# Kernel tuning notes

Measured on AMD Instinct MI355X. Metric: run time of the kernel, lower is better.

The kernel has to match this reference:

```python
import jax, jax.numpy as jnp
import numpy as np

B, S, D, H = 2, 2048, 1024, 16
DK = D // H


def setup_inputs() -> dict:
    key = jax.random.key(0)
    ks = jax.random.split(key, 12)
    scale = 1.0 / np.sqrt(D)
    inp = {
        "q": jax.random.normal(ks[0], (B, S, D), jnp.float32),
        "k": jax.random.normal(ks[1], (B, S, D), jnp.float32),
        "v": jax.random.normal(ks[2], (B, S, D), jnp.float32),
        # causal mask: 1 = attend, 0 = mask, broadcastable to (B, 1, S, S)
        "mask": jnp.tril(jnp.ones((S, S), jnp.int32))[None, None, :, :],
        "Wq": jax.random.normal(ks[3], (D, D), jnp.float32) * scale,
        "bq": jax.random.normal(ks[4], (D,), jnp.float32) * scale,
        "Wk": jax.random.normal(ks[5], (D, D), jnp.float32) * scale,
        "bk": jax.random.normal(ks[6], (D,), jnp.float32) * scale,
        "Wv": jax.random.normal(ks[7], (D, D), jnp.float32) * scale,
        "bv": jax.random.normal(ks[8], (D,), jnp.float32) * scale,
        "Wo": jax.random.normal(ks[9], (D, D), jnp.float32) * scale,
        "bo": jax.random.normal(ks[10], (D,), jnp.float32) * scale,
    }
    return inp


def _split_heads(x):
    b, s, _ = x.shape
    return x.reshape(b, s, H, DK).transpose(0, 2, 1, 3)  # (b, h, s, dk)


def reference(q, k, v, mask, Wq, bq, Wk, bk, Wv, bv, Wo, bo):
    Q = _split_heads(q @ Wq.T + bq)
    K = _split_heads(k @ Wk.T + bk)
    V = _split_heads(v @ Wv.T + bv)
    scores = jnp.einsum("bhqd,bhkd->bhqk", Q, K) * (DK ** -0.5)
    scores = jnp.where(mask == 0, -jnp.inf, scores)
    attn = jax.nn.softmax(scores, axis=-1)  # dropout p=0.0 -> identity
    out = jnp.einsum("bhqk,bhkd->bhqd", attn, V)
    out = out.transpose(0, 2, 1, 3).reshape(q.shape[0], q.shape[1], D)
    return out @ Wo.T + bo
```

## Files before the change

### kernel.cpp

```cpp
#include <hip/hip_runtime.h>


#define S_LEN 2048
#define NHEAD 16
#define DMODEL 1024
#define DKH 64
#define LDT 88

typedef unsigned short u16;
typedef __attribute__((ext_vector_type(4))) short short4v;
typedef __attribute__((ext_vector_type(8))) short short8;
typedef __attribute__((ext_vector_type(8))) __bf16 bf16x8;
typedef __attribute__((ext_vector_type(4))) float f32x4;

__device__ inline u16 f2bf(float f) {
  return __builtin_bit_cast(u16, (__bf16)f);
}

__device__ inline f32x4 mfma16x16(bf16x8 a, bf16x8 b, f32x4 c) {
  return __builtin_amdgcn_mfma_f32_16x16x32_bf16(a, b, c, 0, 0, 0);
}

__device__ inline short8 pack8(float4 a, float4 b) {
  short8 r;
  r[0] = (short)f2bf(a.x); r[1] = (short)f2bf(a.y);
  r[2] = (short)f2bf(a.z); r[3] = (short)f2bf(a.w);
  r[4] = (short)f2bf(b.x); r[5] = (short)f2bf(b.y);
  r[6] = (short)f2bf(b.z); r[7] = (short)f2bf(b.w);
  return r;
}

typedef const __attribute__((address_space(1))) unsigned GU32;
typedef __attribute__((address_space(3))) unsigned LU32;
__device__ inline void gl2lds16(const void* g, void* l) {
  __builtin_amdgcn_global_load_lds((GU32*)g, (LU32*)l, 16, 0, 0);
}

#define SWZ(row, col8) (((row) * 8 + ((col8) ^ ((row) & 7))) * 8)

__global__ __launch_bounds__(256)
void conv_w(const float* __restrict__ w0, const float* __restrict__ w1,
            const float* __restrict__ w2, const float* __restrict__ w3,
            u16* __restrict__ o0, u16* __restrict__ o1,
            u16* __restrict__ o2, u16* __restrict__ o3)
{
  const int z = blockIdx.y;
  const float* s = z == 0 ? w0 : z == 1 ? w1 : z == 2 ? w2 : w3;
  u16* d = z == 0 ? o0 : z == 1 ? o1 : z == 2 ? o2 : o3;
  const int i = (blockIdx.x * 256 + threadIdx.x) * 8;
  float4 a = *(const float4*)&s[i];
  float4 b = *(const float4*)&s[i + 4];
  *(short8*)&d[i] = pack8(a, b);
}

__global__ __launch_bounds__(256)
void proj_gemm(const float* __restrict__ Aq, const float* __restrict__ Akk,
               const float* __restrict__ Av,
               const u16* __restrict__ Bq, const u16* __restrict__ Bk,
               const u16* __restrict__ Bv,
               const float* __restrict__ cq, const float* __restrict__ ck,
               const float* __restrict__ cv,
               u16* __restrict__ Oq, u16* __restrict__ Ok, u16* __restrict__ Ov)
{
  __shared__ u16 SM[3 * 128 * 64];
  u16* As = SM;
  u16* Bs0 = SM + 8192;
  u16* Bs1 = SM + 16384;

  const int hw = blockIdx.x + (blockIdx.y << 3) + (blockIdx.z << 8);
  const int xcd = hw & 7, sq = hw >> 3;
  const int pan = sq % 12, xb = sq / 12;
  const int p = pan * 8 + xcd;
  const int zz = p >> 5, py = p & 31;

  const float* Af = zz == 0 ? Aq : zz == 1 ? Akk : Av;
  const u16* Wb = zz == 0 ? Bq : zz == 1 ? Bk : Bv;
  const float* bias = zz == 0 ? cq : zz == 1 ? ck : cv;

  const int t = threadIdx.x;
  const int lane = t & 63;
  const int wv = t >> 6;
  const int wm = wv >> 1, wn = wv & 1;
  const int g = lane >> 4, lr = lane & 15;
  const int bm = py << 7, bn = xb << 7;
  const int K = DMODEL;

  float4 ax[4], ay[4];
  auto ALOAD = [&](int kt) {
    const int k0 = kt << 6;
#pragma unroll
    for (int i = 0; i < 4; ++i) {
      int c = t + (i << 8);
      int row = c >> 3, col8 = c & 7;
      const float* src = &Af[(size_t)(bm + row) * K + k0 + col8 * 8];
      ax[i] = *(const float4*)src;
      ay[i] = *(const float4*)(src + 4);
    }
  };
  auto AWRITE = [&]() {
#pragma unroll
    for (int i = 0; i < 4; ++i) {
      int c = t + (i << 8);
      int row = c >> 3, col8 = c & 7;
      *(short8*)&As[SWZ(row, col8)] = pack8(ax[i], ay[i]);
    }
  };
  auto BSTAGE = [&](u16* buf, int kt) {
    const int k0 = kt << 6;
#pragma unroll
    for (int i = 0; i < 4; ++i) {
      int c = t + (i << 8);
      int row = c >> 3, col8 = c & 7;
      int c8s = col8 ^ (row & 7);
      gl2lds16(&Wb[(size_t)(bn + row) * K + k0 + c8s * 8], &buf[c * 8]);
    }
  };

  f32x4 acc[4][4] = {};
  ALOAD(0);
  BSTAGE(Bs0, 0);
  AWRITE();
  __syncthreads();
  for (int kt = 0; kt < 16; ++kt) {
    u16* Bcur = (kt & 1) ? Bs1 : Bs0;
    u16* Bnxt = (kt & 1) ? Bs0 : Bs1;
    const bool more = (kt + 1 < 16);
    if (more) { ALOAD(kt + 1); BSTAGE(Bnxt, kt + 1); }
    bf16x8 af[2][4], bf[2][4];
#pragma unroll
    for (int kc = 0; kc < 2; ++kc)
#pragma unroll
      for (int f = 0; f < 4; ++f) {
        af[kc][f] = *(const bf16x8*)&As[SWZ(wm * 64 + f * 16 + lr, kc * 4 + g)];
        bf[kc][f] = *(const bf16x8*)&Bcur[SWZ(wn * 64 + f * 16 + lr, kc * 4 + g)];
      }
#pragma unroll
    for (int kc = 0; kc < 2; ++kc)
#pragma unroll
      for (int fm = 0; fm < 4; ++fm)
#pragma unroll
        for (int fn = 0; fn < 4; ++fn)
          acc[fm][fn] = mfma16x16(af[kc][fm], bf[kc][fn], acc[fm][fn]);
    __syncthreads();
    if (more) {
      AWRITE();
      __syncthreads();
    }
  }

  if (zz == 2) {
    u16* TL = SM;
    const int b = bm >> 11, s0 = bm & (S_LEN - 1), h0 = bn >> 6;
#pragma unroll
    for (int hh = 0; hh < 2; ++hh) {
      __syncthreads();
      if (wn == hh) {
#pragma unroll
        for (int fm = 0; fm < 4; ++fm)
#pragma unroll
          for (int fn = 0; fn < 4; ++fn) {
            const int lch = fn * 16 + lr;
            const float bb = bias[bn + hh * 64 + lch];
#pragma unroll
            for (int r = 0; r < 4; ++r)
              TL[lch * 132 + wm * 64 + fm * 16 + g * 4 + r] = f2bf(acc[fm][fn][r] + bb);
          }
      }
      __syncthreads();
#pragma unroll
      for (int i = 0; i < 4; ++i) {
        int c = t + (i << 8);
        int dk = c >> 4, sc = (c & 15) << 3;
        short8 vv = *(const short8*)&TL[dk * 132 + sc];
        *(short8*)&Ov[(((size_t)(b * NHEAD + h0 + hh)) * DKH + dk) * S_LEN + s0 + sc] = vv;
      }
    }
  } else {
    u16* Out = zz == 0 ? Oq : Ok;
#pragma unroll
    for (int fm = 0; fm < 4; ++fm)
#pragma unroll
      for (int fn = 0; fn < 4; ++fn) {
        const int col = bn + wn * 64 + fn * 16 + lr;
        const int h = col >> 6, dk = col & (DKH - 1);
        const float bb = bias[col];
#pragma unroll
        for (int r = 0; r < 4; ++r) {
          const int row = bm + wm * 64 + fm * 16 + g * 4 + r;
          const int b = row >> 11, s = row & (S_LEN - 1);
          Out[(((size_t)(b * NHEAD + h)) * S_LEN + s) * DKH + dk] = f2bf(acc[fm][fn][r] + bb);
        }
      }
  }
}

__global__ __launch_bounds__(256)
void out_gemm(const u16* __restrict__ Ao, const u16* __restrict__ Wb,
              const float* __restrict__ bias, float* __restrict__ Out)
{
  __shared__ u16 SM[4 * 128 * 64];
  const int hw = blockIdx.x + (blockIdx.y << 3);
  const int xcd = hw & 7, sq = hw >> 3;
  const int pan = sq & 3, xb = sq >> 2;
  const int prow = pan * 8 + xcd;

  const int t = threadIdx.x;
  const int lane = t & 63;
  const int wv = t >> 6;
  const int wm = wv >> 1, wn = wv & 1;
  const int g = lane >> 4, lr = lane & 15;
  const int bm = prow << 7, bn = xb << 7;
  const int K = DMODEL;

  auto STAGE = [&](int buf, int kt) {
    const int k0 = kt << 6;
    u16* Asb = SM + buf * 8192;
    u16* Bsb = SM + 16384 + buf * 8192;
#pragma unroll
    for (int i = 0; i < 4; ++i) {
      int c = t + (i << 8);
      int row = c >> 3, col8 = c & 7;
      int c8s = col8 ^ (row & 7);
      int grow = bm + row;
      int b = grow >> 11, s = grow & (S_LEN - 1);
      int k = k0 + c8s * 8;
      int h = k >> 6, dk = k & (DKH - 1);
      gl2lds16(&Ao[(((size_t)(b * NHEAD + h)) * S_LEN + s) * DKH + dk], &Asb[c * 8]);
      gl2lds16(&Wb[(size_t)(bn + row) * K + k0 + c8s * 8], &Bsb[c * 8]);
    }
  };

  f32x4 acc[4][4] = {};
  STAGE(0, 0);
  __syncthreads();
  for (int kt = 0; kt < 16; ++kt) {
    const int cur = kt & 1;
    if (kt + 1 < 16) STAGE(cur ^ 1, kt + 1);
    u16* Asb = SM + cur * 8192;
    u16* Bsb = SM + 16384 + cur * 8192;
    bf16x8 af[2][4], bf[2][4];
#pragma unroll
    for (int kc = 0; kc < 2; ++kc)
#pragma unroll
      for (int f = 0; f < 4; ++f) {
        af[kc][f] = *(const bf16x8*)&Asb[SWZ(wm * 64 + f * 16 + lr, kc * 4 + g)];
        bf[kc][f] = *(const bf16x8*)&Bsb[SWZ(wn * 64 + f * 16 + lr, kc * 4 + g)];
      }
#pragma unroll
    for (int kc = 0; kc < 2; ++kc)
#pragma unroll
      for (int fm = 0; fm < 4; ++fm)
#pragma unroll
        for (int fn = 0; fn < 4; ++fn)
          acc[fm][fn] = mfma16x16(af[kc][fm], bf[kc][fn], acc[fm][fn]);
    __syncthreads();
  }
#pragma unroll
  for (int fm = 0; fm < 4; ++fm)
#pragma unroll
    for (int fn = 0; fn < 4; ++fn) {
      const int col = bn + wn * 64 + fn * 16 + lr;
      const float bb = bias[col];
#pragma unroll
      for (int r = 0; r < 4; ++r) {
        const int row = bm + wm * 64 + fm * 16 + g * 4 + r;
        Out[(size_t)row * DMODEL + col] = acc[fm][fn][r] + bb;
      }
    }
}

template<bool AF32, int OMODE>
__global__ __launch_bounds__(256)
void gemm64(const void* __restrict__ Ap, const float* __restrict__ Bt,
            const float* __restrict__ bias, void* __restrict__ outp,
            int M, int N, int K)
{
  __shared__ u16 As[64 * LDT];
  __shared__ u16 Bs[64 * LDT];
  const int t = threadIdx.x;
  const int lane = t & 63;
  const int wv = t >> 6;
  const int wm = wv >> 1, wn = wv & 1;
  const int g = lane >> 4, lr = lane & 15;
  const int bm = blockIdx.y << 6, bn = blockIdx.x << 6;

  f32x4 acc[2][2] = {};
  const int nk = K >> 6;
  for (int kt = 0; kt < nk; ++kt) {
    const int k0 = kt << 6;
    __syncthreads();
#pragma unroll
    for (int i = 0; i < 2; ++i) {
      int c = t + (i << 8);
      int row = c >> 3, col = (c & 7) << 3;
      short8 av;
      if (AF32) {
        const float* Af = (const float*)Ap;
        const float4* pa = (const float4*)&Af[(size_t)(bm + row) * K + k0 + col];
        av = pack8(pa[0], pa[1]);
      } else {
        av = *(const short8*)&((const u16*)Ap)[(size_t)(bm + row) * K + k0 + col];
      }
      *(short8*)&As[row * LDT + col] = av;
      const float4* pb = (const float4*)&Bt[(size_t)(bn + row) * K + k0 + col];
      *(short8*)&Bs[row * LDT + col] = pack8(pb[0], pb[1]);
    }
    __syncthreads();
    bf16x8 af[2][2], bfr[2][2];
#pragma unroll
    for (int kc = 0; kc < 2; ++kc) {
#pragma unroll
      for (int fm = 0; fm < 2; ++fm)
        af[kc][fm] = *(const bf16x8*)&As[(wm * 32 + fm * 16 + lr) * LDT + kc * 32 + g * 8];
#pragma unroll
      for (int fn = 0; fn < 2; ++fn)
        bfr[kc][fn] = *(const bf16x8*)&Bs[(wn * 32 + fn * 16 + lr) * LDT + kc * 32 + g * 8];
    }
#pragma unroll
    for (int kc = 0; kc < 2; ++kc)
#pragma unroll
      for (int fm = 0; fm < 2; ++fm)
#pragma unroll
        for (int fn = 0; fn < 2; ++fn)
          acc[fm][fn] = mfma16x16(af[kc][fm], bfr[kc][fn], acc[fm][fn]);
  }
  if (OMODE == 2) {
    u16* TL = As;
    __syncthreads();
#pragma unroll
    for (int fm = 0; fm < 2; ++fm)
#pragma unroll
      for (int fn = 0; fn < 2; ++fn) {
        const int lc = wn * 32 + fn * 16 + lr;
        const float bb = bias[bn + lc];
#pragma unroll
        for (int r = 0; r < 4; ++r) {
          const int lrow = wm * 32 + fm * 16 + g * 4 + r;
          TL[lc * LDT + lrow] = f2bf(acc[fm][fn][r] + bb);
        }
      }
    __syncthreads();
    const int bh = (bm >> 11) * NHEAD + (bn >> 6);
    const int s0 = bm & (S_LEN - 1);
#pragma unroll
    for (int i = 0; i < 2; ++i) {
      int c = t + (i << 8);
      int dr = c >> 3, sc = (c & 7) << 3;
      short8 vv = *(const short8*)&TL[dr * LDT + sc];
      *(short8*)&((u16*)outp)[((size_t)bh * DKH + dr) * S_LEN + s0 + sc] = vv;
    }
  } else {
#pragma unroll
    for (int fm = 0; fm < 2; ++fm)
#pragma unroll
      for (int fn = 0; fn < 2; ++fn) {
        const int col = bn + wn * 32 + fn * 16 + lr;
        const float bb = bias[col];
#pragma unroll
        for (int r = 0; r < 4; ++r) {
          const int row = bm + wm * 32 + fm * 16 + g * 4 + r;
          float vv = acc[fm][fn][r] + bb;
          if (OMODE == 1) {
            int b = row >> 11, s = row & (S_LEN - 1);
            int h = col >> 6, dk = col & (DKH - 1);
            ((u16*)outp)[(((size_t)(b * NHEAD + h)) * S_LEN + s) * DKH + dk] = f2bf(vv);
          } else {
            ((float*)outp)[(size_t)row * N + col] = vv;
          }
        }
      }
  }
}

template<bool HS>
__global__ __launch_bounds__(256)
void attn_fwd(const u16* __restrict__ Qh, const u16* __restrict__ Kh,
              const u16* __restrict__ Vtg, u16* __restrict__ Ao)
{
  __shared__ u16 Ks[2][64 * LDT];
  __shared__ u16 Vs[2][64 * LDT];
  __shared__ u16 Ps[8][16 * LDT];
  const int t = threadIdx.x, lane = t & 63, w = t >> 6;
  const int g = lane >> 4, lr = lane & 15;
  const int bh = blockIdx.y;
  const int pA = blockIdx.x;
  const int tA = pA, tB = 31 - pA;
  const u16* Qb = Qh + (size_t)bh * S_LEN * DKH;
  const u16* Kb = Kh + (size_t)bh * S_LEN * DKH;
  const u16* Vb = Vtg + (size_t)bh * DKH * S_LEN;

  bf16x8 qfA[2], qfB[2];
#pragma unroll
  for (int kc = 0; kc < 2; ++kc) {
    qfA[kc] = *(const bf16x8*)&Qb[(size_t)(tA * 64 + w * 16 + lr) * DKH + kc * 32 + g * 8];
    qfB[kc] = *(const bf16x8*)&Qb[(size_t)(tB * 64 + w * 16 + lr) * DKH + kc * 32 + g * 8];
  }

  f32x4 oA[4] = {}, oB[4] = {};
  float mA = -1e30f, lA = 0.f, mB = -1e30f, lB = 0.f;

  const int r0 = t >> 3;
  const int c0 = (t & 7) << 3;
  short8 kr0, kr1, vr0, vr1;

  auto LOADT = [&](int kt) {
    const int kv0 = kt << 6;
    kr0 = *(const short8*)&Kb[(size_t)(kv0 + r0) * DKH + c0];
    kr1 = *(const short8*)&Kb[(size_t)(kv0 + r0 + 32) * DKH + c0];
    vr0 = *(const short8*)&Vb[(size_t)r0 * S_LEN + kv0 + c0];
    vr1 = *(const short8*)&Vb[(size_t)(r0 + 32) * S_LEN + kv0 + c0];
  };
  auto WRITET = [&](int b) {
    *(short8*)&Ks[b][r0 * LDT + c0] = kr0;
    *(short8*)&Ks[b][(r0 + 32) * LDT + c0] = kr1;
    *(short8*)&Vs[b][r0 * LDT + c0] = vr0;
    *(short8*)&Vs[b][(r0 + 32) * LDT + c0] = vr1;
  };

  auto COMPUTE = [&](int buf, const bf16x8* qf, f32x4* o, float& m, float& l,
                     int pslot, bool diag) {
    f32x4 sf[4];
#pragma unroll
    for (int fk = 0; fk < 4; ++fk) {
      f32x4 a = {};
#pragma unroll
      for (int kc = 0; kc < 2; ++kc) {
        bf16x8 kf = *(const bf16x8*)&Ks[buf][(fk * 16 + lr) * LDT + kc * 32 + g * 8];
        a = mfma16x16(kf, qf[kc], a);
      }
      sf[fk] = a;
    }
    if (diag) {
#pragma unroll
      for (int fk = 0; fk < 4; ++fk)
#pragma unroll
        for (int r = 0; r < 4; ++r)
          if (fk * 16 + 4 * g + r > w * 16 + lr) sf[fk][r] = -1e30f;
    }
    float pm = fmaxf(fmaxf(sf[0][0], sf[0][1]), fmaxf(sf[0][2], sf[0][3]));
#pragma unroll
    for (int fk = 1; fk < 4; ++fk)
      pm = fmaxf(pm, fmaxf(fmaxf(sf[fk][0], sf[fk][1]), fmaxf(sf[fk][2], sf[fk][3])));
    pm = fmaxf(pm, __shfl_xor(pm, 16, 64));
    pm = fmaxf(pm, __shfl_xor(pm, 32, 64));
    float alpha = 1.0f;
    if (!__all(pm - m <= 64.0f)) {
      float mn = fmaxf(m, pm);
      alpha = __expf((m - mn) * 0.125f);
      m = mn;
#pragma unroll
      for (int r = 0; r < 4; ++r) {
        float ar = __shfl(alpha, 4 * g + r, 64);
#pragma unroll
        for (int d = 0; d < 4; ++d) o[d][r] *= ar;
      }
    }
    float rs = 0.f;
#pragma unroll
    for (int fk = 0; fk < 4; ++fk) {
      float p0 = __expf((sf[fk][0] - m) * 0.125f);
      float p1 = __expf((sf[fk][1] - m) * 0.125f);
      float p2 = __expf((sf[fk][2] - m) * 0.125f);
      float p3 = __expf((sf[fk][3] - m) * 0.125f);
      rs += (p0 + p1) + (p2 + p3);
      short4v pk;
      pk[0] = (short)f2bf(p0); pk[1] = (short)f2bf(p1);
      pk[2] = (short)f2bf(p2); pk[3] = (short)f2bf(p3);
      *(short4v*)&Ps[pslot][lr * LDT + fk * 16 + 4 * g] = pk;
    }
    rs += __shfl_xor(rs, 16, 64);
    rs += __shfl_xor(rs, 32, 64);
    l = l * alpha + rs;
#pragma unroll
    for (int kc = 0; kc < 2; ++kc) {
      bf16x8 pf = *(const bf16x8*)&Ps[pslot][lr * LDT + kc * 32 + g * 8];
#pragma unroll
      for (int df = 0; df < 4; ++df) {
        bf16x8 vf = *(const bf16x8*)&Vs[buf][(df * 16 + lr) * LDT + kc * 32 + g * 8];
        o[df] = mfma16x16(pf, vf, o[df]);
      }
    }
  };

  const int nt = tB + 1;
  LOADT(0);
  WRITET(0);
  for (int kt = 0; kt < nt; ++kt) {
    const int cur = kt & 1;
    const bool more = (kt + 1 < nt);
    if (more) LOADT(kt + 1);
    __syncthreads();
    if (kt <= tA) COMPUTE(cur, qfA, oA, mA, lA, w, kt == tA);
    COMPUTE(cur, qfB, oB, mB, lB, 4 + w, kt == tB);
    if (more) WRITET(cur ^ 1);
  }

  float iA[4], iB[4];
#pragma unroll
  for (int r = 0; r < 4; ++r) {
    iA[r] = __builtin_amdgcn_rcpf(__shfl(lA, 4 * g + r, 64));
    iB[r] = __builtin_amdgcn_rcpf(__shfl(lB, 4 * g + r, 64));
  }
  const int b = bh >> 4, h = bh & (NHEAD - 1);
#pragma unroll
  for (int df = 0; df < 4; ++df)
#pragma unroll
    for (int r = 0; r < 4; ++r) {
      const int d = df * 16 + lr;
      const int qa = tA * 64 + w * 16 + g * 4 + r;
      const int qb2 = tB * 64 + w * 16 + g * 4 + r;
      if (HS) {
        Ao[((size_t)bh * S_LEN + qa) * DKH + d] = f2bf(oA[df][r] * iA[r]);
        Ao[((size_t)bh * S_LEN + qb2) * DKH + d] = f2bf(oB[df][r] * iB[r]);
      } else {
        Ao[((size_t)(b * S_LEN + qa)) * DMODEL + h * DKH + d] = f2bf(oA[df][r] * iA[r]);
        Ao[((size_t)(b * S_LEN + qb2)) * DMODEL + h * DKH + d] = f2bf(oB[df][r] * iB[r]);
      }
    }
}

extern "C" void kernel_launch(void* const* d_in, const int* in_sizes, int n_in,
                              void* d_out, int out_size, void* d_ws, size_t ws_size,
                              hipStream_t stream)
{
  (void)in_sizes; (void)n_in; (void)out_size;
  const float* q  = (const float*)d_in[0];
  const float* k  = (const float*)d_in[1];
  const float* v  = (const float*)d_in[2];
  const float* Wq = (const float*)d_in[4];
  const float* bq = (const float*)d_in[5];
  const float* Wk = (const float*)d_in[6];
  const float* bk = (const float*)d_in[7];
  const float* Wv = (const float*)d_in[8];
  const float* bv = (const float*)d_in[9];
  const float* Wo = (const float*)d_in[10];
  const float* bo = (const float*)d_in[11];

  char* ws = (char*)d_ws;
  const size_t MB = 1024 * 1024;

  if (ws_size >= 40 * MB) {
    u16* Wqb = (u16*)(ws);
    u16* Wkb = (u16*)(ws + 2 * MB);
    u16* Wvb = (u16*)(ws + 4 * MB);
    u16* Wob = (u16*)(ws + 6 * MB);
    u16* Qh  = (u16*)(ws + 8 * MB);
    u16* Kh  = (u16*)(ws + 16 * MB);
    u16* Vt  = (u16*)(ws + 24 * MB);
    u16* Ao  = (u16*)(ws + 32 * MB);

    conv_w<<<dim3(512, 4), 256, 0, stream>>>(Wq, Wk, Wv, Wo, Wqb, Wkb, Wvb, Wob);
    proj_gemm<<<dim3(8, 32, 3), 256, 0, stream>>>(q, k, v, Wqb, Wkb, Wvb,
                                                  bq, bk, bv, Qh, Kh, Vt);
    attn_fwd<true><<<dim3(16, 2 * NHEAD), 256, 0, stream>>>(Qh, Kh, Vt, Ao);
    out_gemm<<<dim3(8, 32), 256, 0, stream>>>(Ao, Wob, bo, (float*)d_out);
  } else {
    u16* Qh = (u16*)(ws);
    u16* Kh = (u16*)(ws + 8 * MB);
    u16* Vt = (u16*)(ws + 16 * MB);
    u16* Ao = (u16*)(ws + 24 * MB);
    const int M = 2 * S_LEN, N = DMODEL, K = DMODEL;
    dim3 gg(N / 64, M / 64), bb(256);
    gemm64<true, 1><<<gg, bb, 0, stream>>>(q, Wq, bq, Qh, M, N, K);
    gemm64<true, 1><<<gg, bb, 0, stream>>>(k, Wk, bk, Kh, M, N, K);
    gemm64<true, 2><<<gg, bb, 0, stream>>>(v, Wv, bv, Vt, M, N, K);
    attn_fwd<false><<<dim3(16, 2 * NHEAD), bb, 0, stream>>>(Qh, Kh, Vt, Ao);
    gemm64<false, 0><<<gg, bb, 0, stream>>>(Ao, Wo, bo, d_out, M, N, K);
  }
}
```

Measured before the change: 131.7 us.

## Pre-convert activations to bf16 and use async LDS-loading projection GEMM

```diff
diff --git a/kernel.cpp b/kernel.cpp
--- a/kernel.cpp
+++ b/kernel.cpp
@@ -37,6 +37,33 @@
 }
 
 #define SWZ(row, col8) (((row) * 8 + ((col8) ^ ((row) & 7))) * 8)
+
+__global__ __launch_bounds__(256)
+void conv_bf16(const float* __restrict__ w0, const float* __restrict__ w1,
+               const float* __restrict__ w2, const float* __restrict__ w3,
+               const float* __restrict__ aq, const float* __restrict__ ak,
+               const float* __restrict__ av,
+               u16* __restrict__ o0, u16* __restrict__ o1,
+               u16* __restrict__ o2, u16* __restrict__ o3,
+               u16* __restrict__ oq, u16* __restrict__ ok, u16* __restrict__ ov)
+{
+  const int y = blockIdx.y;
+  const float* s; u16* d; int n;
+  switch (y) {
+    case 0: s = w0; d = o0; n = 1 << 20; break;
+    case 1: s = w1; d = o1; n = 1 << 20; break;
+    case 2: s = w2; d = o2; n = 1 << 20; break;
+    case 3: s = w3; d = o3; n = 1 << 20; break;
+    case 4: s = aq; d = oq; n = 1 << 22; break;
+    case 5: s = ak; d = ok; n = 1 << 22; break;
+    default: s = av; d = ov; n = 1 << 22; break;
+  }
+  const int i = (blockIdx.x * 256 + threadIdx.x) * 8;
+  if (i >= n) return;
+  float4 a = *(const float4*)&s[i];
+  float4 b = *(const float4*)&s[i + 4];
+  *(short8*)&d[i] = pack8(a, b);
+}
 
 __global__ __launch_bounds__(256)
 void conv_w(const float* __restrict__ w0, const float* __restrict__ w1,
@@ -54,15 +81,130 @@
 }
 
 __global__ __launch_bounds__(256)
-void proj_gemm(const float* __restrict__ Aq, const float* __restrict__ Akk,
-               const float* __restrict__ Av,
-               const u16* __restrict__ Bq, const u16* __restrict__ Bk,
-               const u16* __restrict__ Bv,
-               const float* __restrict__ cq, const float* __restrict__ ck,
-               const float* __restrict__ cv,
-               u16* __restrict__ Oq, u16* __restrict__ Ok, u16* __restrict__ Ov)
+void proj_gemm_bf16(const u16* __restrict__ Aqb, const u16* __restrict__ Akb,
+                    const u16* __restrict__ Avb,
+                    const u16* __restrict__ Bq, const u16* __restrict__ Bk,
+                    const u16* __restrict__ Bv,
+                    const float* __restrict__ cq, const float* __restrict__ ck,
+                    const float* __restrict__ cv,
+                    u16* __restrict__ Oq, u16* __restrict__ Ok, u16* __restrict__ Ov)
 {
-  __shared__ u16 SM[3 * 128 * 64];
+  __shared__ u16 SM[4 * 8192];
+
+  const int hw = blockIdx.x + (blockIdx.y << 3) + (blockIdx.z << 8);
+  const int xcd = hw & 7, sq = hw >> 3;
+  const int pan = sq % 12, xb = sq / 12;
+  const int p = pan * 8 + xcd;
+  const int zz = p >> 5, py = p & 31;
+
+  const u16* Ab = zz == 0 ? Aqb : zz == 1 ? Akb : Avb;
+  const u16* Wb = zz == 0 ? Bq : zz == 1 ? Bk : Bv;
+  const float* bias = zz == 0 ? cq : zz == 1 ? ck : cv;
+
+  const int t = threadIdx.x;
+  const int lane = t & 63;
+  const int wv = t >> 6;
+  const int wm = wv >> 1, wn = wv & 1;
+  const int g = lane >> 4, lr = lane & 15;
+  const int bm = py << 7, bn = xb << 7;
+  const int K = DMODEL;
+
+  auto STAGE = [&](int buf, int kt) {
+    const int k0 = kt << 6;
+    u16* Asb = SM + buf * 8192;
+    u16* Bsb = SM + 16384 + buf * 8192;
+#pragma unroll
+    for (int i = 0; i < 4; ++i) {
+      int c = t + (i << 8);
+      int row = c >> 3, col8 = c & 7;
+      int c8s = col8 ^ (row & 7);
+      gl2lds16(&Ab[(size_t)(bm + row) * K + k0 + c8s * 8], &Asb[c * 8]);
+      gl2lds16(&Wb[(size_t)(bn + row) * K + k0 + c8s * 8], &Bsb[c * 8]);
+    }
+  };
+
+  f32x4 acc[4][4] = {};
+  STAGE(0, 0);
+  __syncthreads();
+  for (int kt = 0; kt < 16; ++kt) {
+    const int cur = kt & 1;
+    if (kt + 1 < 16) STAGE(cur ^ 1, kt + 1);
+    u16* Asb = SM + cur * 8192;
+    u16* Bsb = SM + 16384 + cur * 8192;
+    bf16x8 af[2][4], bf[2][4];
+#pragma unroll
+    for (int kc = 0; kc < 2; ++kc)
+#pragma unroll
+      for (int f = 0; f < 4; ++f) {
+        af[kc][f] = *(const bf16x8*)&Asb[SWZ(wm * 64 + f * 16 + lr, kc * 4 + g)];
+        bf[kc][f] = *(const bf16x8*)&Bsb[SWZ(wn * 64 + f * 16 + lr, kc * 4 + g)];
+      }
+#pragma unroll
+    for (int kc = 0; kc < 2; ++kc)
+#pragma unroll
+      for (int fm = 0; fm < 4; ++fm)
+#pragma unroll
+        for (int fn = 0; fn < 4; ++fn)
+          acc[fm][fn] = mfma16x16(af[kc][fm], bf[kc][fn], acc[fm][fn]);
+    __syncthreads();
+  }
+
+  if (zz == 2) {
+    u16* TL = SM;
+    const int b = bm >> 11, s0 = bm & (S_LEN - 1), h0 = bn >> 6;
+#pragma unroll
+    for (int hh = 0; hh < 2; ++hh) {
+      __syncthreads();
+      if (wn == hh) {
+#pragma unroll
+        for (int fm = 0; fm < 4; ++fm)
+#pragma unroll
+          for (int fn = 0; fn < 4; ++fn) {
+            const int lch = fn * 16 + lr;
+            const float bb = bias[bn + hh * 64 + lch];
+#pragma unroll
+            for (int r = 0; r < 4; ++r)
+              TL[lch * 132 + wm * 64 + fm * 16 + g * 4 + r] = f2bf(acc[fm][fn][r] + bb);
+          }
+      }
+      __syncthreads();
+#pragma unroll
+      for (int i = 0; i < 4; ++i) {
+        int c = t + (i << 8);
+        int dk = c >> 4, sc = (c & 15) << 3;
+        short8 vv = *(const short8*)&TL[dk * 132 + sc];
+        *(short8*)&Ov[(((size_t)(b * NHEAD + h0 + hh)) * DKH + dk) * S_LEN + s0 + sc] = vv;
+      }
+    }
+  } else {
+    u16* Out = zz == 0 ? Oq : Ok;
+#pragma unroll
+    for (int fm = 0; fm < 4; ++fm)
+#pragma unroll
+      for (int fn = 0; fn < 4; ++fn) {
+        const int col = bn + wn * 64 + fn * 16 + lr;
+        const int h = col >> 6, dk = col & (DKH - 1);
+        const float bb = bias[col];
+#pragma unroll
+        for (int r = 0; r < 4; ++r) {
+          const int row = bm + wm * 64 + fm * 16 + g * 4 + r;
+          const int b = row >> 11, s = row & (S_LEN - 1);
+          Out[(((size_t)(b * NHEAD + h)) * S_LEN + s) * DKH + dk] = f2bf(acc[fm][fn][r] + bb);
+        }
+      }
+  }
+}
+
+__global__ __launch_bounds__(256)
+void proj_gemm_f32(const float* __restrict__ Aq, const float* __restrict__ Akk,
+                   const float* __restrict__ Av,
+                   const u16* __restrict__ Bq, const u16* __restrict__ Bk,
+                   const u16* __restrict__ Bv,
+                   const float* __restrict__ cq, const float* __restrict__ ck,
+                   const float* __restrict__ cv,
+                   u16* __restrict__ Oq, u16* __restrict__ Ok, u16* __restrict__ Ov)
+{
+  __shared__ u16 SM[3 * 8192];
   u16* As = SM;
   u16* Bs0 = SM + 8192;
   u16* Bs1 = SM + 16384;
@@ -198,7 +340,7 @@
 void out_gemm(const u16* __restrict__ Ao, const u16* __restrict__ Wb,
               const float* __restrict__ bias, float* __restrict__ Out)
 {
-  __shared__ u16 SM[4 * 128 * 64];
+  __shared__ u16 SM[4 * 8192];
   const int hw = blockIdx.x + (blockIdx.y << 3);
   const int xcd = hw & 7, sq = hw >> 3;
   const int pan = sq & 3, xb = sq >> 2;
@@ -269,110 +411,6 @@
     }
 }
 
-template<bool AF32, int OMODE>
-__global__ __launch_bounds__(256)
-void gemm64(const void* __restrict__ Ap, const float* __restrict__ Bt,
-            const float* __restrict__ bias, void* __restrict__ outp,
-            int M, int N, int K)
-{
-  __shared__ u16 As[64 * LDT];
-  __shared__ u16 Bs[64 * LDT];
-  const int t = threadIdx.x;
-  const int lane = t & 63;
-  const int wv = t >> 6;
-  const int wm = wv >> 1, wn = wv & 1;
-  const int g = lane >> 4, lr = lane & 15;
-  const int bm = blockIdx.y << 6, bn = blockIdx.x << 6;
-
-  f32x4 acc[2][2] = {};
-  const int nk = K >> 6;
-  for (int kt = 0; kt < nk; ++kt) {
-    const int k0 = kt << 6;
-    __syncthreads();
-#pragma unroll
-    for (int i = 0; i < 2; ++i) {
-      int c = t + (i << 8);
-      int row = c >> 3, col = (c & 7) << 3;
-      short8 av;
-      if (AF32) {
-        const float* Af = (const float*)Ap;
-        const float4* pa = (const float4*)&Af[(size_t)(bm + row) * K + k0 + col];
-        av = pack8(pa[0], pa[1]);
-      } else {
-        av = *(const short8*)&((const u16*)Ap)[(size_t)(bm + row) * K + k0 + col];
-      }
-      *(short8*)&As[row * LDT + col] = av;
-      const float4* pb = (const float4*)&Bt[(size_t)(bn + row) * K + k0 + col];
-      *(short8*)&Bs[row * LDT + col] = pack8(pb[0], pb[1]);
-    }
-    __syncthreads();
-    bf16x8 af[2][2], bfr[2][2];
-#pragma unroll
-    for (int kc = 0; kc < 2; ++kc) {
-#pragma unroll
-      for (int fm = 0; fm < 2; ++fm)
-        af[kc][fm] = *(const bf16x8*)&As[(wm * 32 + fm * 16 + lr) * LDT + kc * 32 + g * 8];
-#pragma unroll
-      for (int fn = 0; fn < 2; ++fn)
-        bfr[kc][fn] = *(const bf16x8*)&Bs[(wn * 32 + fn * 16 + lr) * LDT + kc * 32 + g * 8];
-    }
-#pragma unroll
-    for (int kc = 0; kc < 2; ++kc)
-#pragma unroll
-      for (int fm = 0; fm < 2; ++fm)
-#pragma unroll
-        for (int fn = 0; fn < 2; ++fn)
-          acc[fm][fn] = mfma16x16(af[kc][fm], bfr[kc][fn], acc[fm][fn]);
-  }
-  if (OMODE == 2) {
-    u16* TL = As;
-    __syncthreads();
-#pragma unroll
-    for (int fm = 0; fm < 2; ++fm)
-#pragma unroll
-      for (int fn = 0; fn < 2; ++fn) {
-        const int lc = wn * 32 + fn * 16 + lr;
-        const float bb = bias[bn + lc];
-#pragma unroll
-        for (int r = 0; r < 4; ++r) {
-          const int lrow = wm * 32 + fm * 16 + g * 4 + r;
-          TL[lc * LDT + lrow] = f2bf(acc[fm][fn][r] + bb);
-        }
-      }
-    __syncthreads();
-    const int bh = (bm >> 11) * NHEAD + (bn >> 6);
-    const int s0 = bm & (S_LEN - 1);
-#pragma unroll
-    for (int i = 0; i < 2; ++i) {
-      int c = t + (i << 8);
-      int dr = c >> 3, sc = (c & 7) << 3;
-      short8 vv = *(const short8*)&TL[dr * LDT + sc];
-      *(short8*)&((u16*)outp)[((size_t)bh * DKH + dr) * S_LEN + s0 + sc] = vv;
-    }
-  } else {
-#pragma unroll
-    for (int fm = 0; fm < 2; ++fm)
-#pragma unroll
-      for (int fn = 0; fn < 2; ++fn) {
-        const int col = bn + wn * 32 + fn * 16 + lr;
-        const float bb = bias[col];
-#pragma unroll
-        for (int r = 0; r < 4; ++r) {
-          const int row = bm + wm * 32 + fm * 16 + g * 4 + r;
-          float vv = acc[fm][fn][r] + bb;
-          if (OMODE == 1) {
-            int b = row >> 11, s = row & (S_LEN - 1);
-            int h = col >> 6, dk = col & (DKH - 1);
-            ((u16*)outp)[(((size_t)(b * NHEAD + h)) * S_LEN + s) * DKH + dk] = f2bf(vv);
-          } else {
-            ((float*)outp)[(size_t)row * N + col] = vv;
-          }
-        }
-      }
-  }
-}
-
-template<bool HS>
 __global__ __launch_bounds__(256)
 void attn_fwd(const u16* __restrict__ Qh, const u16* __restrict__ Kh,
               const u16* __restrict__ Vtg, u16* __restrict__ Ao)
@@ -501,7 +539,6 @@
     iA[r] = __builtin_amdgcn_rcpf(__shfl(lA, 4 * g + r, 64));
     iB[r] = __builtin_amdgcn_rcpf(__shfl(lB, 4 * g + r, 64));
   }
-  const int b = bh >> 4, h = bh & (NHEAD - 1);
 #pragma unroll
   for (int df = 0; df < 4; ++df)
 #pragma unroll
@@ -509,13 +546,8 @@
       const int d = df * 16 + lr;
       const int qa = tA * 64 + w * 16 + g * 4 + r;
       const int qb2 = tB * 64 + w * 16 + g * 4 + r;
-      if (HS) {
-        Ao[((size_t)bh * S_LEN + qa) * DKH + d] = f2bf(oA[df][r] * iA[r]);
-        Ao[((size_t)bh * S_LEN + qb2) * DKH + d] = f2bf(oB[df][r] * iB[r]);
-      } else {
-        Ao[((size_t)(b * S_LEN + qa)) * DMODEL + h * DKH + d] = f2bf(oA[df][r] * iA[r]);
-        Ao[((size_t)(b * S_LEN + qb2)) * DMODEL + h * DKH + d] = f2bf(oB[df][r] * iB[r]);
-      }
+      Ao[((size_t)bh * S_LEN + qa) * DKH + d] = f2bf(oA[df][r] * iA[r]);
+      Ao[((size_t)bh * S_LEN + qb2) * DKH + d] = f2bf(oB[df][r] * iB[r]);
     }
 }
 
@@ -539,7 +571,26 @@
   char* ws = (char*)d_ws;
   const size_t MB = 1024 * 1024;
 
-  if (ws_size >= 40 * MB) {
+  if (ws_size >= 56 * MB) {
+    u16* Wqb = (u16*)(ws);
+    u16* Wkb = (u16*)(ws + 2 * MB);
+    u16* Wvb = (u16*)(ws + 4 * MB);
+    u16* Wob = (u16*)(ws + 6 * MB);
+    u16* qb  = (u16*)(ws + 8 * MB);
+    u16* kb  = (u16*)(ws + 16 * MB);
+    u16* vb  = (u16*)(ws + 24 * MB);
+    u16* Qh  = (u16*)(ws + 32 * MB);
+    u16* Kh  = (u16*)(ws + 40 * MB);
+    u16* Vt  = (u16*)(ws + 48 * MB);
+    u16* Ao  = qb;
+
+    conv_bf16<<<dim3(2048, 7), 256, 0, stream>>>(Wq, Wk, Wv, Wo, q, k, v,
+                                                 Wqb, Wkb, Wvb, Wob, qb, kb, vb);
+    proj_gemm_bf16<<<dim3(8, 32, 3), 256, 0, stream>>>(qb, kb, vb, Wqb, Wkb, Wvb,
+                                                       bq, bk, bv, Qh, Kh, Vt);
+    attn_fwd<<<dim3(16, 2 * NHEAD), 256, 0, stream>>>(Qh, Kh, Vt, Ao);
+    out_gemm<<<dim3(8, 32), 256, 0, stream>>>(Ao, Wob, bo, (float*)d_out);
+  } else {
     u16* Wqb = (u16*)(ws);
     u16* Wkb = (u16*)(ws + 2 * MB);
     u16* Wvb = (u16*)(ws + 4 * MB);
@@ -550,21 +601,9 @@
     u16* Ao  = (u16*)(ws + 32 * MB);
 
     conv_w<<<dim3(512, 4), 256, 0, stream>>>(Wq, Wk, Wv, Wo, Wqb, Wkb, Wvb, Wob);
-    proj_gemm<<<dim3(8, 32, 3), 256, 0, stream>>>(q, k, v, Wqb, Wkb, Wvb,
-                                                  bq, bk, bv, Qh, Kh, Vt);
-    attn_fwd<true><<<dim3(16, 2 * NHEAD), 256, 0, stream>>>(Qh, Kh, Vt, Ao);
+    proj_gemm_f32<<<dim3(8, 32, 3), 256, 0, stream>>>(q, k, v, Wqb, Wkb, Wvb,
+                                                      bq, bk, bv, Qh, Kh, Vt);
+    attn_fwd<<<dim3(16, 2 * NHEAD), 256, 0, stream>>>(Qh, Kh, Vt, Ao);
     out_gemm<<<dim3(8, 32), 256, 0, stream>>>(Ao, Wob, bo, (float*)d_out);
-  } else {
-    u16* Qh = (u16*)(ws);
-    u16* Kh = (u16*)(ws + 8 * MB);
-    u16* Vt = (u16*)(ws + 16 * MB);
-    u16* Ao = (u16*)(ws + 24 * MB);
-    const int M = 2 * S_LEN, N = DMODEL, K = DMODEL;
-    dim3 gg(N / 64, M / 64), bb(256);
-    gemm64<true, 1><<<gg, bb, 0, stream>>>(q, Wq, bq, Qh, M, N, K);
-    gemm64<true, 1><<<gg, bb, 0, stream>>>(k, Wk, bk, Kh, M, N, K);
-    gemm64<true, 2><<<gg, bb, 0, stream>>>(v, Wv, bv, Vt, M, N, K);
-    attn_fwd<false><<<dim3(16, 2 * NHEAD), bb, 0, stream>>>(Qh, Kh, Vt, Ao);
-    gemm64<false, 0><<<gg, bb, 0, stream>>>(Ao, Wo, bo, d_out, M, N, K);
-  }
-}
+  }
+}
```

New measurement: 120.6 us (median of 3 runs). -8.4%, faster.
